# Optimization experiments

Hardware: AMD Instinct MI355X
Metric: run time of the kernel (lower is better)

Reference implementation:

```python
import jax, jax.numpy as jnp
import numpy as np

ALPHA = 0.2          # LeakyReLU negative slope
BIG_NEG = -9e15      # mask value used by the torch module
N, FT, C = 8192, 512, 64


def setup_inputs() -> dict:
    key = jax.random.key(0)
    ks = jax.random.split(key, 7)
    features = jax.random.normal(ks[0], (N, FT), jnp.float32)
    W = jax.random.normal(ks[1], (FT, C), jnp.float32) * (1.0 / np.sqrt(FT))
    a = jax.random.normal(ks[2], (2 * C, 1), jnp.float32) * 0.1
    adj1 = jax.random.randint(ks[3], (N, N), 0, 2, jnp.int32)
    adj2 = jax.random.randint(ks[4], (N, N), 0, 2, jnp.int32)
    labels = jax.random.randint(ks[5], (N,), 0, C, jnp.int32)
    idx_train = jax.random.randint(ks[6], (1024,), 0, N, jnp.int32)
    return dict(features=features, W=W, a=a, adj1=adj1, adj2=adj2,
                labels=labels, idx_train=idx_train)


def _gat_layer(h, adj, W, a):
    # Wh: [N, C]
    Wh = h @ W
    c = W.shape[1]
    # The torch code builds an [N, N, 2C] cat tensor then does @ a.
    # That is exactly e_ij = leaky_relu(Wh_i . a[:C] + Wh_j . a[C:]),
    # so compute the two rank-1 terms and broadcast-add instead.
    src = Wh @ a[:c]          # [N, 1] contribution of row node i
    dst = Wh @ a[c:]          # [N, 1] contribution of col node j
    e = jax.nn.leaky_relu(src + dst.T, ALPHA)          # [N, N]
    attn = jax.nn.softmax(jnp.where(adj > 0, e, BIG_NEG), axis=1)
    # dropout is identity in eval mode
    return jax.nn.elu(attn @ Wh)                        # concat=True -> elu


def reference(features, W, a, adj1, adj2, labels, idx_train):
    h_all = jnp.stack(
        [jax.nn.relu(_gat_layer(features, adj, W, a)) for adj in (adj1, adj2)],
        axis=0,
    ).mean(axis=0)                                      # [N, C]
    logits = h_all[idx_train]                           # [n_train, C]
    logp = jax.nn.log_softmax(logits, axis=-1)
    y = labels[idx_train]
    loss = -jnp.take_along_axis(logp, y[:, None], axis=1).mean()
    return loss
```

## Files before the change

### kernel.cpp

```cpp
#include <hip/hip_runtime.h>
#include <hip/hip_bf16.h>


#define NN 8192
#define FTDIM 512
#define CDIM 64
#define NTRAIN 1024
#define LOG2E 1.44269504088896f

typedef __attribute__((ext_vector_type(8))) short short8;
typedef __attribute__((ext_vector_type(4))) float f32x4;
typedef __attribute__((ext_vector_type(4))) int i32x4;

static __device__ __forceinline__ unsigned short f2bf(float x) {
    return __bfloat16_as_ushort(__float2bfloat16(x));
}
static __device__ __forceinline__ float bf2f(unsigned short u) {
    return __uint_as_float((unsigned)u << 16);
}

__global__ __launch_bounds__(256) void k_prep(
    const float* __restrict__ W, unsigned short* __restrict__ Wt2,
    float* __restrict__ out)
{
    if (blockIdx.x == 0 && threadIdx.x == 0) out[0] = 0.f;
    const int idx0 = blockIdx.x * 256 + threadIdx.x;
    for (int idx = idx0; idx < 64 * 64; idx += 16 * 256) {
        const int kblk = idx >> 6, c = idx & 63;
        short8 v;
#pragma unroll
        for (int e = 0; e < 8; ++e)
            v[e] = (short)f2bf(W[(kblk * 8 + e) * CDIM + c]);
        *(short8*)(Wt2 + (size_t)idx * 8) = v;
    }
}

__global__ __launch_bounds__(64) void k_wh(
    const float* __restrict__ feat, const unsigned short* __restrict__ Wt2,
    const float* __restrict__ av, unsigned short* __restrict__ Vt2,
    float4* __restrict__ sQ, float* __restrict__ dE1, float* __restrict__ dE2)
{
    const int lane = threadIdx.x;
    const int r  = lane & 15;
    const int kg = lane >> 4;
    const int row0 = blockIdx.x * 16;

    const float* __restrict__ fp = feat + (size_t)(row0 + r) * FTDIM + kg * 8;

    f32x4 fa[4], fb[4];
#pragma unroll
    for (int d = 0; d < 4; ++d) {
        fa[d] = *(const f32x4*)(fp + d * 32);
        fb[d] = *(const f32x4*)(fp + d * 32 + 4);
    }

    f32x4 acc0 = {0.f, 0.f, 0.f, 0.f};
    f32x4 acc1 = acc0, acc2 = acc0, acc3 = acc0;

    for (int it = 0; it < 16; ++it) {
        const int slot = it & 3;
        const f32x4 a0 = fa[slot], a1 = fb[slot];
        if (it + 4 < 16) {
            fa[slot] = *(const f32x4*)(fp + (it + 4) * 32);
            fb[slot] = *(const f32x4*)(fp + (it + 4) * 32 + 4);
        }

        short8 af;
#pragma unroll
        for (int e = 0; e < 4; ++e) {
            af[e]     = (short)f2bf(a0[e]);
            af[4 + e] = (short)f2bf(a1[e]);
        }

        const unsigned short* bp = Wt2 + ((size_t)(it * 4 + kg)) * 512 + (r << 3);
        const short8 b0 = *(const short8*)(bp);
        const short8 b1 = *(const short8*)(bp + 128);
        const short8 b2 = *(const short8*)(bp + 256);
        const short8 b3 = *(const short8*)(bp + 384);

        acc0 = __builtin_amdgcn_mfma_f32_16x16x32_bf16(af, b0, acc0, 0, 0, 0);
        acc1 = __builtin_amdgcn_mfma_f32_16x16x32_bf16(af, b1, acc1, 0, 0, 0);
        acc2 = __builtin_amdgcn_mfma_f32_16x16x32_bf16(af, b2, acc2, 0, 0, 0);
        acc3 = __builtin_amdgcn_mfma_f32_16x16x32_bf16(af, b3, acc3, 0, 0, 0);
    }

    const size_t jblk = (size_t)(row0 >> 3) + (kg >> 1);
    const int e0 = (kg & 1) * 4;
#pragma unroll
    for (int nt = 0; nt < 4; ++nt) {
        const f32x4 a = (nt == 0) ? acc0 : (nt == 1) ? acc1 : (nt == 2) ? acc2 : acc3;
        ushort4 v4;
        v4.x = f2bf(a[0]); v4.y = f2bf(a[1]); v4.z = f2bf(a[2]); v4.w = f2bf(a[3]);
        *(ushort4*)(Vt2 + jblk * 512 + (size_t)(nt * 16 + r) * 8 + e0) = v4;
    }

    float a1v[4], a2v[4];
#pragma unroll
    for (int nt = 0; nt < 4; ++nt) {
        a1v[nt] = av[nt * 16 + r];
        a2v[nt] = av[CDIM + nt * 16 + r];
    }
#pragma unroll
    for (int q = 0; q < 4; ++q) {
        float s_ = acc0[q] * a1v[0] + acc1[q] * a1v[1]
                 + acc2[q] * a1v[2] + acc3[q] * a1v[3];
        float d_ = acc0[q] * a2v[0] + acc1[q] * a2v[1]
                 + acc2[q] * a2v[2] + acc3[q] * a2v[3];
#pragma unroll
        for (int off = 8; off; off >>= 1) {
            s_ += __shfl_xor(s_, off);
            d_ += __shfl_xor(d_, off);
        }
        if (r == 0) {
            const int i = row0 + kg * 4 + q;
            const float sp = s_ * LOG2E, dp_ = d_ * LOG2E;
            sQ[i] = make_float4(__builtin_amdgcn_exp2f(sp),
                                __builtin_amdgcn_exp2f(0.2f * sp),
                                __builtin_amdgcn_exp2f(-sp), 0.f);
            dE1[i] = __builtin_amdgcn_exp2f(dp_);
            dE2[i] = __builtin_amdgcn_exp2f(0.2f * dp_);
        }
    }
}

struct TileS {
    f32x4 a0, a1, b0, b1;
    short8 v0, v1, v2, v3;
};

template<int SCL>
__global__ __launch_bounds__(256, 4) void k_mattn(
    const int* __restrict__ adj1, const int* __restrict__ adj2,
    const unsigned short* __restrict__ Vt2, const float4* __restrict__ sQ,
    const float* __restrict__ dE1, const float* __restrict__ dE2,
    const int* __restrict__ idxt,
    unsigned short* __restrict__ numPartB, float* __restrict__ zPart)
{
    constexpr int NT = (NN >> SCL) >> 5;
    const int lane = threadIdx.x & 63;
    const int w = (int)((blockIdx.x * blockDim.x + threadIdx.x) >> 6);
    const int l   = w >> (6 + SCL);
    const int rem = w & ((64 << SCL) - 1);
    const int sc  = rem >> 6;
    const int sb  = rem & 63;

    const int r  = lane & 15;
    const int kg = lane >> 4;

    const int i = idxt[sb * 16 + r];
    const float4 sq = sQ[i];
    const float E1 = sq.x, E2 = sq.y, th = sq.z;

    const int j0 = sc * (NN >> SCL);
    const int* __restrict__ arow = (l ? adj2 : adj1) + (size_t)i * NN + j0 + kg * 8;
    const float* __restrict__ d1p = dE1 + j0 + kg * 8;
    const float* __restrict__ d2p = dE2 + j0 + kg * 8;
    const unsigned short* __restrict__ vbase =
        Vt2 + (((size_t)j0 >> 3) << 9) + ((size_t)kg << 9) + (r << 3);

    unsigned mbits[NT];
#pragma unroll
    for (int g = 0; g < NT; g += 4) {
        i32x4 gm0[4], gm1[4];
#pragma unroll
        for (int t = 0; t < 4; ++t) {
            gm0[t] = *(const i32x4*)(arow + (g + t) * 32);
            gm1[t] = *(const i32x4*)(arow + (g + t) * 32 + 4);
        }
#pragma unroll
        for (int t = 0; t < 4; ++t) {
            unsigned m = 0;
#pragma unroll
            for (int e = 0; e < 4; ++e) {
                m |= (gm0[t][e] != 0 ? 1u : 0u) << e;
                m |= (gm1[t][e] != 0 ? 1u : 0u) << (4 + e);
            }
            mbits[g + t] = m;
        }
    }

    short8 bOnes;
#pragma unroll
    for (int e = 0; e < 8; ++e) bOnes[e] = (short)0x3F80;

    f32x4 acc0 = {0.f, 0.f, 0.f, 0.f};
    f32x4 acc1 = acc0, acc2 = acc0, acc3 = acc0, accz = acc0;

    TileS tA, tB;

#define LOADT(T, JT) do { const int _jr = (JT) * 32;                           \
    T.a0 = *(const f32x4*)(d1p + _jr);                                         \
    T.a1 = *(const f32x4*)(d1p + _jr + 4);                                     \
    T.b0 = *(const f32x4*)(d2p + _jr);                                         \
    T.b1 = *(const f32x4*)(d2p + _jr + 4);                                     \
    const unsigned short* _vp = vbase + ((size_t)(JT) << 11);                  \
    T.v0 = *(const short8*)(_vp);                                              \
    T.v1 = *(const short8*)(_vp + 128);                                        \
    T.v2 = *(const short8*)(_vp + 256);                                        \
    T.v3 = *(const short8*)(_vp + 384);                                        \
} while (0)

#define COMPT(T, JT) do {                                                      \
    const unsigned _mb = mbits[JT];                                            \
    short8 af;                                                                 \
    _Pragma("unroll")                                                          \
    for (int e = 0; e < 8; ++e) {                                              \
        const float e1 = (e < 4) ? T.a0[e & 3] : T.a1[e & 3];                  \
        const float e2 = (e < 4) ? T.b0[e & 3] : T.b1[e & 3];                  \
        const bool pos = e1 > th;                                              \
        float p = (pos ? e1 : e2) * (pos ? E1 : E2);                           \
        p = ((_mb >> e) & 1u) ? p : 0.f;                                       \
        af[e] = (short)f2bf(p);                                                \
    }                                                                          \
    acc0 = __builtin_amdgcn_mfma_f32_16x16x32_bf16(af, T.v0, acc0, 0, 0, 0);   \
    acc1 = __builtin_amdgcn_mfma_f32_16x16x32_bf16(af, T.v1, acc1, 0, 0, 0);   \
    acc2 = __builtin_amdgcn_mfma_f32_16x16x32_bf16(af, T.v2, acc2, 0, 0, 0);   \
    acc3 = __builtin_amdgcn_mfma_f32_16x16x32_bf16(af, T.v3, acc3, 0, 0, 0);   \
    accz = __builtin_amdgcn_mfma_f32_16x16x32_bf16(af, bOnes, accz, 0, 0, 0);  \
} while (0)

    LOADT(tA, 0);
#pragma unroll
    for (int jt = 0; jt < NT - 2; jt += 2) {
        LOADT(tB, jt + 1);
        COMPT(tA, jt);
        LOADT(tA, jt + 2);
        COMPT(tB, jt + 1);
    }
    LOADT(tB, NT - 1);
    COMPT(tA, NT - 2);
    COMPT(tB, NT - 1);
#undef LOADT
#undef COMPT

    constexpr int SC = 1 << SCL;
#pragma unroll
    for (int q = 0; q < 4; ++q) {
        const int ks = sb * 16 + kg * 4 + q;
        const size_t slot = ((size_t)ks * 2 + l) * SC + sc;
        unsigned short* op = numPartB + slot * CDIM + r;
        op[0]  = f2bf(acc0[q]);
        op[16] = f2bf(acc1[q]);
        op[32] = f2bf(acc2[q]);
        op[48] = f2bf(acc3[q]);
        if (r == 0) zPart[slot] = accz[q];
    }
}

__global__ __launch_bounds__(256) void k_loss(
    const unsigned short* __restrict__ numPartB, const float* __restrict__ zPart,
    const int* __restrict__ labels, const int* __restrict__ idxt,
    float* __restrict__ out, const int scLog2)
{
    __shared__ float lsum[4];
    const int tid = threadIdx.x;
    const int lane = tid & 63;
    const int wv = tid >> 6;
    const int k = (int)((blockIdx.x * blockDim.x + tid) >> 6);
    const int SC = 1 << scLog2;

    float logit = 0.f;
#pragma unroll
    for (int l = 0; l < 2; ++l) {
        const size_t base = ((size_t)k * 2 + l) * SC;
        float ns = 0.f;
#pragma unroll 16
        for (int s = 0; s < SC; ++s)
            ns += bf2f(numPartB[(base + s) * CDIM + lane]);
        float zs = (lane < SC) ? zPart[base + lane] : 0.f;
#pragma unroll
        for (int off = 32; off; off >>= 1) zs += __shfl_xor(zs, off);
        logit += fmaxf(ns / zs, 0.f);
    }
    logit *= 0.5f;

    float m = logit;
#pragma unroll
    for (int off = 32; off; off >>= 1) m = fmaxf(m, __shfl_xor(m, off));
    float ex = __expf(logit - m);
    float sum = ex;
#pragma unroll
    for (int off = 32; off; off >>= 1) sum += __shfl_xor(sum, off);
    const float logp = logit - m - __logf(sum);

    const int y = labels[idxt[k]];
    const float t = __shfl(logp, y);
    if (lane == 0) lsum[wv] = -t;
    __syncthreads();
    if (tid == 0)
        atomicAdd(out, (lsum[0] + lsum[1] + lsum[2] + lsum[3]) * (1.f / 1024.f));
}

extern "C" void kernel_launch(void* const* d_in, const int* in_sizes, int n_in,
                              void* d_out, int out_size, void* d_ws, size_t ws_size,
                              hipStream_t stream)
{
    const float* feat   = (const float*)d_in[0];
    const float* W      = (const float*)d_in[1];
    const float* av     = (const float*)d_in[2];
    const int*   adj1   = (const int*)d_in[3];
    const int*   adj2   = (const int*)d_in[4];
    const int*   labels = (const int*)d_in[5];
    const int*   idxt   = (const int*)d_in[6];

    const size_t HEAD = (1u << 20) + (256u << 10);

    auto needed = [&](int scl) -> size_t {
        const size_t SC = (size_t)1 << scl;
        return HEAD + 2 * SC * NTRAIN * CDIM * sizeof(unsigned short)
                    + 2 * SC * NTRAIN * sizeof(float);
    };
    const int scLog2 = (ws_size >= needed(5)) ? 5 : 4;
    const int SC = 1 << scLog2;

    char* ws = (char*)d_ws;
    unsigned short* Vt2 = (unsigned short*)ws;
    unsigned short* Wt2 = (unsigned short*)(ws + (1u << 20));
    float4* sQ  = (float4*)(ws + (1u << 20) + (64u << 10));
    float*  dE1 = (float*)(ws + (1u << 20) + (192u << 10));
    float*  dE2 = (float*)(ws + (1u << 20) + (224u << 10));
    unsigned short* numPartB = (unsigned short*)(ws + HEAD);
    float*  zPart  = (float*)((char*)numPartB
                              + 2ull * SC * NTRAIN * CDIM * sizeof(unsigned short));

    hipLaunchKernelGGL(k_prep, dim3(16), dim3(256), 0, stream,
                       W, Wt2, (float*)d_out);
    hipLaunchKernelGGL(k_wh, dim3(512), dim3(64), 0, stream,
                       feat, Wt2, av, Vt2, sQ, dE1, dE2);
    if (scLog2 == 5)
        hipLaunchKernelGGL((k_mattn<5>), dim3(32 * 32), dim3(256), 0, stream,
                           adj1, adj2, Vt2, sQ, dE1, dE2, idxt, numPartB, zPart);
    else
        hipLaunchKernelGGL((k_mattn<4>), dim3(32 * 16), dim3(256), 0, stream,
                           adj1, adj2, Vt2, sQ, dE1, dE2, idxt, numPartB, zPart);
    hipLaunchKernelGGL(k_loss, dim3(NTRAIN / 4), dim3(256), 0, stream,
                       numPartB, zPart, labels, idxt, (float*)d_out, scLog2);
}
```

Before: 43.46 us.

## Pack adjacency rows into bitmask in separate pass merged with W prep

Adds a pass, merged with the W-to-bf16 prep kernel, that reads the 2x1024 gathered adjacency rows once with fully coalesced wide loads and compresses them into a bitmask in workspace. The attention kernel then reads packed 64-bit mask words instead of strided int32 adjacency values, which removes scattered global loads from its prologue and leaves fewer registers live. The total adjacency bytes read stay the same, but now in a bandwidth-friendly pattern. The cost is a small extra workspace buffer, an extra write and read of the mask, and a wider prep launch before k_wh.

```diff
diff --git a/kernel.cpp b/kernel.cpp
--- a/kernel.cpp
+++ b/kernel.cpp
@@ -19,19 +19,52 @@
     return __uint_as_float((unsigned)u << 16);
 }
 
-__global__ __launch_bounds__(256) void k_prep(
-    const float* __restrict__ W, unsigned short* __restrict__ Wt2,
+__global__ __launch_bounds__(256) void k_madj(
+    const int* __restrict__ adj1, const int* __restrict__ adj2,
+    const int* __restrict__ idxt, const float* __restrict__ W,
+    unsigned short* __restrict__ Wt2, unsigned short* __restrict__ maskB,
     float* __restrict__ out)
 {
-    if (blockIdx.x == 0 && threadIdx.x == 0) out[0] = 0.f;
-    const int idx0 = blockIdx.x * 256 + threadIdx.x;
-    for (int idx = idx0; idx < 64 * 64; idx += 16 * 256) {
+    const int tid = threadIdx.x;
+
+    if (blockIdx.x < 16) {
+        const int idx = blockIdx.x * 256 + tid;
         const int kblk = idx >> 6, c = idx & 63;
         short8 v;
 #pragma unroll
         for (int e = 0; e < 8; ++e)
             v[e] = (short)f2bf(W[(kblk * 8 + e) * CDIM + c]);
         *(short8*)(Wt2 + (size_t)idx * 8) = v;
+        if (blockIdx.x == 0 && tid == 0) out[0] = 0.f;
+    }
+
+    const int lane = tid & 63;
+    const int w2   = blockIdx.x * 4 + (tid >> 6);
+    const int half = w2 & 1;
+    const int row  = w2 >> 1;
+    const int l    = row >> 10;
+    const int ks   = row & 1023;
+    const int i    = idxt[ks];
+
+    const int* __restrict__ arow = (l ? adj2 : adj1) + (size_t)i * NN + half * 4096;
+    unsigned short* __restrict__ mrow = maskB + (size_t)row * 512 + half * 256;
+
+#pragma unroll
+    for (int u = 0; u < 4; ++u) {
+        const int lb = u * 1024 + lane * 16;
+        const i32x4 a0 = *(const i32x4*)(arow + lb);
+        const i32x4 a1 = *(const i32x4*)(arow + lb + 4);
+        const i32x4 a2 = *(const i32x4*)(arow + lb + 8);
+        const i32x4 a3 = *(const i32x4*)(arow + lb + 12);
+        unsigned m = 0;
+#pragma unroll
+        for (int e = 0; e < 4; ++e) {
+            m |= (a0[e] != 0 ? 1u : 0u) << e;
+            m |= (a1[e] != 0 ? 1u : 0u) << (4 + e);
+            m |= (a2[e] != 0 ? 1u : 0u) << (8 + e);
+            m |= (a3[e] != 0 ? 1u : 0u) << (12 + e);
+        }
+        mrow[u * 64 + lane] = (unsigned short)m;
     }
 }
 
@@ -130,7 +163,7 @@
 
 template<int SCL>
 __global__ __launch_bounds__(256, 4) void k_mattn(
-    const int* __restrict__ adj1, const int* __restrict__ adj2,
+    const unsigned short* __restrict__ maskB,
     const unsigned short* __restrict__ Vt2, const float4* __restrict__ sQ,
     const float* __restrict__ dE1, const float* __restrict__ dE2,
     const int* __restrict__ idxt,
@@ -147,37 +180,28 @@
     const int r  = lane & 15;
     const int kg = lane >> 4;
 
-    const int i = idxt[sb * 16 + r];
+    const int ks = sb * 16 + r;
+    const int i = idxt[ks];
     const float4 sq = sQ[i];
     const float E1 = sq.x, E2 = sq.y, th = sq.z;
 
     const int j0 = sc * (NN >> SCL);
-    const int* __restrict__ arow = (l ? adj2 : adj1) + (size_t)i * NN + j0 + kg * 8;
     const float* __restrict__ d1p = dE1 + j0 + kg * 8;
     const float* __restrict__ d2p = dE2 + j0 + kg * 8;
     const unsigned short* __restrict__ vbase =
         Vt2 + (((size_t)j0 >> 3) << 9) + ((size_t)kg << 9) + (r << 3);
 
+    const unsigned long long* __restrict__ mptr =
+        (const unsigned long long*)((const char*)maskB
+            + (size_t)((l << 10) + ks) * 1024 + (j0 >> 3));
+    unsigned long long mw[NT / 2];
+#pragma unroll
+    for (int ww = 0; ww < NT / 2; ++ww) mw[ww] = mptr[ww];
+
     unsigned mbits[NT];
 #pragma unroll
-    for (int g = 0; g < NT; g += 4) {
-        i32x4 gm0[4], gm1[4];
-#pragma unroll
-        for (int t = 0; t < 4; ++t) {
-            gm0[t] = *(const i32x4*)(arow + (g + t) * 32);
-            gm1[t] = *(const i32x4*)(arow + (g + t) * 32 + 4);
-        }
-#pragma unroll
-        for (int t = 0; t < 4; ++t) {
-            unsigned m = 0;
-#pragma unroll
-            for (int e = 0; e < 4; ++e) {
-                m |= (gm0[t][e] != 0 ? 1u : 0u) << e;
-                m |= (gm1[t][e] != 0 ? 1u : 0u) << (4 + e);
-            }
-            mbits[g + t] = m;
-        }
-    }
+    for (int t = 0; t < NT; ++t)
+        mbits[t] = (unsigned)(mw[t >> 1] >> (((t & 1) * 4 + kg) * 8)) & 0xffu;
 
     short8 bOnes;
 #pragma unroll
@@ -236,8 +260,8 @@
     constexpr int SC = 1 << SCL;
 #pragma unroll
     for (int q = 0; q < 4; ++q) {
-        const int ks = sb * 16 + kg * 4 + q;
-        const size_t slot = ((size_t)ks * 2 + l) * SC + sc;
+        const int kss = sb * 16 + kg * 4 + q;
+        const size_t slot = ((size_t)kss * 2 + l) * SC + sc;
         unsigned short* op = numPartB + slot * CDIM + r;
         op[0]  = f2bf(acc0[q]);
         op[16] = f2bf(acc1[q]);
@@ -303,7 +327,8 @@
     const int*   labels = (const int*)d_in[5];
     const int*   idxt   = (const int*)d_in[6];
 
-    const size_t HEAD = (1u << 20) + (256u << 10);
+    const size_t MASKB = 2ull * NTRAIN * (NN / 8);
+    const size_t HEAD  = (1u << 20) + (256u << 10) + MASKB;
 
     auto needed = [&](int scl) -> size_t {
         const size_t SC = (size_t)1 << scl;
@@ -319,20 +344,21 @@
     float4* sQ  = (float4*)(ws + (1u << 20) + (64u << 10));
     float*  dE1 = (float*)(ws + (1u << 20) + (192u << 10));
     float*  dE2 = (float*)(ws + (1u << 20) + (224u << 10));
+    unsigned short* maskB = (unsigned short*)(ws + (1u << 20) + (256u << 10));
     unsigned short* numPartB = (unsigned short*)(ws + HEAD);
     float*  zPart  = (float*)((char*)numPartB
                               + 2ull * SC * NTRAIN * CDIM * sizeof(unsigned short));
 
-    hipLaunchKernelGGL(k_prep, dim3(16), dim3(256), 0, stream,
-                       W, Wt2, (float*)d_out);
+    hipLaunchKernelGGL(k_madj, dim3(1024), dim3(256), 0, stream,
+                       adj1, adj2, idxt, W, Wt2, maskB, (float*)d_out);
     hipLaunchKernelGGL(k_wh, dim3(512), dim3(64), 0, stream,
                        feat, Wt2, av, Vt2, sQ, dE1, dE2);
     if (scLog2 == 5)
         hipLaunchKernelGGL((k_mattn<5>), dim3(32 * 32), dim3(256), 0, stream,
-                           adj1, adj2, Vt2, sQ, dE1, dE2, idxt, numPartB, zPart);
+                           maskB, Vt2, sQ, dE1, dE2, idxt, numPartB, zPart);
     else
         hipLaunchKernelGGL((k_mattn<4>), dim3(32 * 16), dim3(256), 0, stream,
-                           adj1, adj2, Vt2, sQ, dE1, dE2, idxt, numPartB, zPart);
+                           maskB, Vt2, sQ, dE1, dE2, idxt, numPartB, zPart);
     hipLaunchKernelGGL(k_loss, dim3(NTRAIN / 4), dim3(256), 0, stream,
                        numPartB, zPart, labels, idxt, (float*)d_out, scLog2);
 }
```

Result: faster. 42.24 us (median of 2 runs) (-2.8%).
